# Optimization experiments

Measured on AMD Instinct MI355X. Metric: run time of the kernel, lower is better.

Reference implementation:

```python
import jax, jax.numpy as jnp
import numpy as np

L, B, E = 2048, 4, 1024
H = 8
D1 = 2048          # expand_ratio * E, multiple of H
HD = D1 // H       # head dim 256
MAX_L = 2048
EPS = 1e-8


def setup_inputs() -> dict:
    key = jax.random.key(0)
    ks = jax.random.split(key, 9)
    std = 0.02
    return {
        "x": jax.random.normal(ks[0], (L, B, E), jnp.float32),
        "Wu": jax.random.normal(ks[1], (D1, E), jnp.float32) * std,
        "bu": jax.random.normal(ks[2], (D1,), jnp.float32) * std,
        "Wv": jax.random.normal(ks[3], (D1, E), jnp.float32) * std,
        "bv": jax.random.normal(ks[4], (D1,), jnp.float32) * std,
        "Wo": jax.random.normal(ks[5], (E, D1), jnp.float32) * std,
        "bo": jax.random.normal(ks[6], (E,), jnp.float32) * std,
        "zero": jax.random.normal(ks[7], (H, 1), jnp.float32) * 0.1,   # Toeplitz coef, offset 0
        "pos": jax.random.normal(ks[8], (H, MAX_L - 1), jnp.float32) * 0.1,  # offsets 1..n-1
    }


def _simple_rmsnorm(x):
    d = x.shape[-1]
    rms = jnp.linalg.norm(x, axis=-1, keepdims=True) * (d ** -0.5)
    return x / (rms + EPS)


def _toeplitz_causal_fft(v, zero, pos):
    # v: (b, h, n, hd); causal Toeplitz mixing along n via FFT long conv
    n = v.shape[-2]
    coef = jnp.concatenate([zero, pos[:, : n - 1]], axis=-1)  # (h, n)
    m = 2 * n
    cf = jnp.fft.rfft(coef, m, axis=-1)                  # (h, m//2+1)
    vf = jnp.fft.rfft(v, m, axis=-2)                     # (b, h, m//2+1, hd)
    out = jnp.fft.irfft(cf[None, :, :, None] * vf, m, axis=-2)
    return out[:, :, :n, :]


def reference(x, Wu, bu, Wv, bv, Wo, bo, zero, pos):
    # x: (n, b, e) fairseq layout
    n, b, e = x.shape
    shortcut = x
    xn = _simple_rmsnorm(x)                               # pre_norm (SimpleRMSNorm, no params)
    u = jax.nn.silu(jnp.einsum('nbe,de->nbd', xn, Wu) + bu)   # (n,b,d1)
    v = jax.nn.silu(jnp.einsum('nbe,de->nbd', xn, Wv) + bv)   # (n,b,d1)
    # 'n b (h d) -> b h n d'
    vh = v.transpose(1, 0, 2).reshape(b, n, H, HD).transpose(0, 2, 1, 3)
    oh = _toeplitz_causal_fft(vh, zero, pos)              # (b,h,n,hd)
    o = oh.transpose(0, 2, 1, 3).reshape(b, n, D1).transpose(1, 0, 2)  # (n,b,d1)
    o = u * o                                             # gating
    out = jnp.einsum('nbd,ed->nbe', o, Wo) + bo + shortcut
    return out
```

## Files before the change

kernel.cpp:

```cpp
#include <hip/hip_runtime.h>
#include <cstdint>
#include <cstddef>

#define LQ   2048
#define BQ   4
#define EQ   1024
#define HQ   8
#define D1Q  2048
#define HDQ  256
#define NBQ  (LQ*BQ)

typedef __bf16 bf16_t;
typedef __bf16 bf16x8 __attribute__((ext_vector_type(8)));
typedef __bf16 bf16x4 __attribute__((ext_vector_type(4)));
typedef float  f32x4  __attribute__((ext_vector_type(4)));

#define GAS1(p) ((const __attribute__((address_space(1))) void*)(p))
#define LAS3(p) ((__attribute__((address_space(3))) void*)(p))


__global__ __launch_bounds__(256) void convert_kernel(
    const float* __restrict__ Wu, const float* __restrict__ Wv,
    const float* __restrict__ Wo,
    bf16_t* __restrict__ Wub, bf16_t* __restrict__ Wvb,
    bf16_t* __restrict__ Wob)
{
    const size_t i = (size_t)blockIdx.x * 256 + threadIdx.x;
    if (i < (size_t)D1Q * EQ) {
        Wub[i] = (bf16_t)Wu[i];
        Wvb[i] = (bf16_t)Wv[i];
        Wob[i] = (bf16_t)Wo[i];
    }
}

__global__ __launch_bounds__(256) void build_toep_tiles(
    const float* __restrict__ zero, const float* __restrict__ pos,
    bf16_t* __restrict__ Atiles)
{
    const int q = blockIdx.x;
    const int h = blockIdx.y;
    const int doff = (q - 3) * 32;
    const int tid = threadIdx.x;
    bf16_t* dst = Atiles + ((size_t)h * 64 + q) * (128 * 32);
    const int e0 = tid * 16;
    const int r = e0 >> 5;
    const int cbase = e0 & 31;
    bf16_t vals[16];
    #pragma unroll
    for (int j = 0; j < 16; ++j) {
        const int d = doff + r - (cbase + j);
        float v = 0.f;
        if (d == 0) v = zero[h];
        else if (d > 0) v = pos[(size_t)h * (LQ - 1) + d - 1];
        vals[j] = (bf16_t)v;
    }
    *(bf16x8*)(dst + e0)     = *(bf16x8*)(vals);
    *(bf16x8*)(dst + e0 + 8) = *(bf16x8*)(vals + 8);
}

__global__ __launch_bounds__(256) void rmsnorm_kernel(
    const float* __restrict__ x, bf16_t* __restrict__ xn)
{
    const int row = blockIdx.x;
    const int tid = threadIdx.x;
    const float4 v = ((const float4*)(x + (size_t)row * EQ))[tid];
    float ss = v.x*v.x + v.y*v.y + v.z*v.z + v.w*v.w;
    #pragma unroll
    for (int m = 32; m >= 1; m >>= 1) ss += __shfl_xor(ss, m, 64);
    __shared__ float red[4];
    const int wid = tid >> 6, lane = tid & 63;
    if (lane == 0) red[wid] = ss;
    __syncthreads();
    const float tot = red[0] + red[1] + red[2] + red[3];
    const float inv = 1.f / (sqrtf(tot * (1.f / EQ)) + 1e-8f);
    bf16x4 o;
    o[0] = (bf16_t)(v.x * inv); o[1] = (bf16_t)(v.y * inv);
    o[2] = (bf16_t)(v.z * inv); o[3] = (bf16_t)(v.w * inv);
    *(bf16x4*)(xn + (size_t)row * EQ + tid * 4) = o;
}

__global__ __launch_bounds__(512, 4) void gemm_uv(
    const bf16_t* __restrict__ A, const bf16_t* __restrict__ Bm,
    const float* __restrict__ bbu, const float* __restrict__ bbv,
    bf16_t* __restrict__ Ub, bf16_t* __restrict__ Vt)
{
    constexpr int K = EQ;
    constexpr int BUF = 24576;
    __shared__ alignas(16) char smem[2 * BUF];

    const int nwg   = gridDim.x * gridDim.y;
    const int bid0  = blockIdx.y * gridDim.x + blockIdx.x;
    const int chunkw = nwg >> 3;
    const int sb    = (bid0 & 7) * chunkw + (bid0 >> 3);
    const int bx    = sb % gridDim.x;
    const int by    = sb / gridDim.x;

    const int tid  = threadIdx.x;
    const int wid  = tid >> 6;
    const int lane = tid & 63;
    const int frow = lane & 15;
    const int c    = lane >> 4;
    const int m0 = by * 256;
    const int n0 = bx * 128;
    const int wm = wid >> 1, wn = wid & 1;
    const int wrm = wm * 64, wrn = wn * 64;

    const int g = (frow >> 1) & 3;
    const int offA0 = (wrm + frow) * 64 + ((c ^ g) << 4);
    const int offB0 = 16384 + (wrn + frow) * 64 + ((c ^ g) << 4);

    const int rA   = tid >> 2;
    const int soff = (((tid & 3) ^ ((rA >> 1) & 3)) << 4);
    const size_t lda2 = (size_t)K * 2;
    const char* sA = (const char*)A  + (size_t)(m0 + rA) * lda2 + soff;
    const char* sB = (const char*)Bm + (size_t)(n0 + rA) * lda2 + soff;

    auto STAGE = [&](int bf, int kt) {
        char* dA = smem + bf * BUF + wid * 1024;
        __builtin_amdgcn_global_load_lds(GAS1(sA + (size_t)kt * 64), LAS3(dA), 16, 0, 0);
        __builtin_amdgcn_global_load_lds(GAS1(sA + 128 * lda2 + (size_t)kt * 64),
                                         LAS3(dA + 8192), 16, 0, 0);
        char* dB = smem + bf * BUF + 16384 + wid * 1024;
        __builtin_amdgcn_global_load_lds(GAS1(sB + (size_t)kt * 64), LAS3(dB), 16, 0, 0);
    };

    f32x4 acc[4][4];
    #pragma unroll
    for (int i = 0; i < 4; ++i)
        #pragma unroll
        for (int j = 0; j < 4; ++j) acc[i][j] = (f32x4){0.f, 0.f, 0.f, 0.f};

    const int NT = K >> 5;

    STAGE(0, 0);
    asm volatile("s_waitcnt vmcnt(0)" ::: "memory");
    __builtin_amdgcn_s_barrier();

    for (int t = 0; t < NT; ++t) {
        if (t + 1 < NT) STAGE((t + 1) & 1, t + 1);
        const char* base = smem + (t & 1) * BUF;
        bf16x8 av[4], bv[4];
        #pragma unroll
        for (int i = 0; i < 4; ++i) {
            av[i] = *(const bf16x8*)(base + offA0 + i * 1024);
            bv[i] = *(const bf16x8*)(base + offB0 + i * 1024);
        }
        __builtin_amdgcn_s_setprio(1);
        #pragma unroll
        for (int mi = 0; mi < 4; ++mi)
            #pragma unroll
            for (int ni = 0; ni < 4; ++ni)
                acc[mi][ni] = __builtin_amdgcn_mfma_f32_16x16x32_bf16(
                    av[mi], bv[ni], acc[mi][ni], 0, 0, 0);
        __builtin_amdgcn_s_setprio(0);
        asm volatile("s_waitcnt vmcnt(0)" ::: "memory");
        __builtin_amdgcn_s_barrier();
    }

    if (bx < 16) {
        const int fq = c * 4;
        #pragma unroll
        for (int mi = 0; mi < 4; ++mi) {
            #pragma unroll
            for (int ni = 0; ni < 4; ++ni) {
                const int gn = n0 + wrn + ni * 16 + frow;
                #pragma unroll
                for (int j = 0; j < 4; ++j) {
                    const int gm = m0 + wrm + mi * 16 + fq + j;
                    float v = acc[mi][ni][j] + bbu[gn];
                    v = v / (1.f + __expf(-v));
                    Ub[(size_t)gm * D1Q + gn] = (bf16_t)v;
                }
            }
        }
        return;
    }

    {
        const int n0v = n0 - 2048;
        const int hh  = n0v >> 8;
        const int hdb = (n0v & 255) + wrn;
        float bb[4];
        #pragma unroll
        for (int ni = 0; ni < 4; ++ni) bb[ni] = bbv[n0v + wrn + ni * 16 + frow];

        bf16_t* chunk = (bf16_t*)smem + wn * 8448;
        #pragma unroll
        for (int p = 0; p < 2; ++p) {
            __syncthreads();
            #pragma unroll
            for (int mi = 0; mi < 4; ++mi) {
                #pragma unroll
                for (int nio = 0; nio < 2; ++nio) {
                    const int ni = p * 2 + nio;
                    const int nl = nio * 16 + frow;
                    const int tl = wm * 16 + mi * 4 + c;
                    #pragma unroll
                    for (int j = 0; j < 4; ++j) {
                        float v = acc[mi][ni][j] + bb[ni];
                        v = v / (1.f + __expf(-v));
                        chunk[nl * 264 + j * 64 + tl] = (bf16_t)v;
                    }
                }
            }
            __syncthreads();
            const int nl    = lane & 31;
            const int thalf = lane >> 5;
            const int b2    = wm;
            const int hd    = hdb + p * 32 + nl;
            const int t0    = (m0 >> 2) + thalf * 32;
            const bf16_t* src = chunk + nl * 264 + b2 * 64 + thalf * 32;
            bf16_t* dst = Vt + (((size_t)hh * 4 + b2) * 256 + hd) * (size_t)LQ + t0;
            #pragma unroll
            for (int u = 0; u < 4; ++u)
                *(bf16x8*)(dst + u * 8) = *(const bf16x8*)(src + u * 8);
        }
    }
}

__global__ __launch_bounds__(256, 4) void gemm_toep(
    const bf16_t* __restrict__ VT, const bf16_t* __restrict__ Atiles,
    const bf16_t* __restrict__ U, bf16_t* __restrict__ O)
{
    constexpr int BUF = 16384;
    __shared__ alignas(16) char smem[2 * BUF];

    const int bid   = blockIdx.x;
    const int m_blk = 15 - (bid >> 6);
    const int sub   = bid & 63;
    const int h     = sub >> 3;
    const int n0    = (sub & 7) * 128;
    const int m0    = m_blk * 128;

    const int tid  = threadIdx.x;
    const int wid  = tid >> 6;
    const int lane = tid & 63;
    const int frow = lane & 15;
    const int c    = lane >> 4;
    const int wm = wid >> 1, wn = wid & 1;
    const int wrm = wm * 64, wrn = wn * 64;

    const int g = (frow >> 1) & 3;
    const int offA0 = (wrm + frow) * 64 + ((c ^ g) << 4);
    const int offB0 = 8192 + (wrn + frow) * 64 + ((c ^ g) << 4);

    const int rA   = tid >> 2;
    const int soff = (((tid & 3) ^ ((rA >> 1) & 3)) << 4);
    const char* Ah = (const char*)Atiles + (size_t)h * 64 * 8192;
    const size_t ldb = (size_t)LQ * 2;
    const char* sB = (const char*)VT + ((size_t)h * 1024 + n0 + rA) * ldb + soff;

    auto STAGE = [&](int bf, int kt) {
        const int q = 4 * m_blk + 3 - kt;
        const char* s = Ah + (size_t)q * 8192 + (size_t)rA * 64 + soff;
        char* dA = smem + bf * BUF + wid * 1024;
        __builtin_amdgcn_global_load_lds(GAS1(s), LAS3(dA), 16, 0, 0);
        __builtin_amdgcn_global_load_lds(GAS1(s + 4096), LAS3(dA + 4096), 16, 0, 0);
        char* dB = smem + bf * BUF + 8192 + wid * 1024;
        __builtin_amdgcn_global_load_lds(GAS1(sB + (size_t)kt * 64), LAS3(dB), 16, 0, 0);
        __builtin_amdgcn_global_load_lds(GAS1(sB + 64 * ldb + (size_t)kt * 64),
                                         LAS3(dB + 4096), 16, 0, 0);
    };

    f32x4 acc[4][4];
    #pragma unroll
    for (int i = 0; i < 4; ++i)
        #pragma unroll
        for (int j = 0; j < 4; ++j) acc[i][j] = (f32x4){0.f, 0.f, 0.f, 0.f};

    const int NT = 4 * m_blk + 4;

    STAGE(0, 0);
    asm volatile("s_waitcnt vmcnt(0)" ::: "memory");
    __builtin_amdgcn_s_barrier();

    for (int t = 0; t < NT; ++t) {
        if (t + 1 < NT) STAGE((t + 1) & 1, t + 1);
        const char* base = smem + (t & 1) * BUF;
        bf16x8 av[4], bv[4];
        #pragma unroll
        for (int i = 0; i < 4; ++i) {
            av[i] = *(const bf16x8*)(base + offA0 + i * 1024);
            bv[i] = *(const bf16x8*)(base + offB0 + i * 1024);
        }
        __builtin_amdgcn_s_setprio(1);
        #pragma unroll
        for (int mi = 0; mi < 4; ++mi)
            #pragma unroll
            for (int ni = 0; ni < 4; ++ni)
                acc[mi][ni] = __builtin_amdgcn_mfma_f32_16x16x32_bf16(
                    av[mi], bv[ni], acc[mi][ni], 0, 0, 0);
        __builtin_amdgcn_s_setprio(0);
        asm volatile("s_waitcnt vmcnt(0)" ::: "memory");
        __builtin_amdgcn_s_barrier();
    }

    const int fq = c * 4;
    #pragma unroll
    for (int mi = 0; mi < 4; ++mi) {
        #pragma unroll
        for (int ni = 0; ni < 4; ++ni) {
            const int nn = n0 + wrn + ni * 16 + frow;
            const int b  = nn >> 8, hd = nn & 255;
            #pragma unroll
            for (int j = 0; j < 4; ++j) {
                const int t = m0 + wrm + mi * 16 + fq + j;
                const size_t idx = ((size_t)t * BQ + b) * D1Q + h * HDQ + hd;
                const float uval = (float)U[idx];
                O[idx] = (bf16_t)(uval * acc[mi][ni][j]);
            }
        }
    }
}

__global__ __launch_bounds__(256, 4) void gemm_fin(
    const bf16_t* __restrict__ A, const bf16_t* __restrict__ Bm,
    const float* __restrict__ bias, const float* __restrict__ res,
    float* __restrict__ Cf)
{
    constexpr int K = D1Q, N = EQ;
    constexpr int BUF = 16384;
    __shared__ alignas(16) char smem[2 * BUF];

    const int nwg   = gridDim.x * gridDim.y;
    const int bid0  = blockIdx.y * gridDim.x + blockIdx.x;
    const int chunkw = nwg >> 3;
    const int sb    = (bid0 & 7) * chunkw + (bid0 >> 3);
    const int bx    = sb % gridDim.x;
    const int by    = sb / gridDim.x;

    const int tid  = threadIdx.x;
    const int wid  = tid >> 6;
    const int lane = tid & 63;
    const int frow = lane & 15;
    const int c    = lane >> 4;
    const int m0 = by * 128;
    const int n0 = bx * 128;
    const int wm = wid >> 1, wn = wid & 1;
    const int wrm = wm * 64, wrn = wn * 64;

    const int g = (frow >> 1) & 3;
    const int offA0 = (wrm + frow) * 64 + ((c ^ g) << 4);
    const int offB0 = 8192 + (wrn + frow) * 64 + ((c ^ g) << 4);

    const int rA   = tid >> 2;
    const int soff = (((tid & 3) ^ ((rA >> 1) & 3)) << 4);
    const size_t lda2 = (size_t)K * 2;
    const char* sA = (const char*)A  + (size_t)(m0 + rA) * lda2 + soff;
    const char* sB = (const char*)Bm + (size_t)(n0 + rA) * lda2 + soff;

    auto STAGE = [&](int bf, int kt) {
        char* dA = smem + bf * BUF + wid * 1024;
        __builtin_amdgcn_global_load_lds(GAS1(sA + (size_t)kt * 64), LAS3(dA), 16, 0, 0);
        __builtin_amdgcn_global_load_lds(GAS1(sA + 64 * lda2 + (size_t)kt * 64),
                                         LAS3(dA + 4096), 16, 0, 0);
        char* dB = smem + bf * BUF + 8192 + wid * 1024;
        __builtin_amdgcn_global_load_lds(GAS1(sB + (size_t)kt * 64), LAS3(dB), 16, 0, 0);
        __builtin_amdgcn_global_load_lds(GAS1(sB + 64 * lda2 + (size_t)kt * 64),
                                         LAS3(dB + 4096), 16, 0, 0);
    };

    f32x4 acc[4][4];
    #pragma unroll
    for (int i = 0; i < 4; ++i)
        #pragma unroll
        for (int j = 0; j < 4; ++j) acc[i][j] = (f32x4){0.f, 0.f, 0.f, 0.f};

    const int NT = K >> 5;

    STAGE(0, 0);
    asm volatile("s_waitcnt vmcnt(0)" ::: "memory");
    __builtin_amdgcn_s_barrier();

    for (int t = 0; t < NT; ++t) {
        if (t + 1 < NT) STAGE((t + 1) & 1, t + 1);
        const char* base = smem + (t & 1) * BUF;
        bf16x8 av[4], bv[4];
        #pragma unroll
        for (int i = 0; i < 4; ++i) {
            av[i] = *(const bf16x8*)(base + offA0 + i * 1024);
            bv[i] = *(const bf16x8*)(base + offB0 + i * 1024);
        }
        __builtin_amdgcn_s_setprio(1);
        #pragma unroll
        for (int mi = 0; mi < 4; ++mi)
            #pragma unroll
            for (int ni = 0; ni < 4; ++ni)
                acc[mi][ni] = __builtin_amdgcn_mfma_f32_16x16x32_bf16(
                    av[mi], bv[ni], acc[mi][ni], 0, 0, 0);
        __builtin_amdgcn_s_setprio(0);
        asm volatile("s_waitcnt vmcnt(0)" ::: "memory");
        __builtin_amdgcn_s_barrier();
    }

    const int fq = c * 4;
    #pragma unroll
    for (int mi = 0; mi < 4; ++mi) {
        #pragma unroll
        for (int ni = 0; ni < 4; ++ni) {
            const int gn = n0 + wrn + ni * 16 + frow;
            #pragma unroll
            for (int j = 0; j < 4; ++j) {
                const int gm = m0 + wrm + mi * 16 + fq + j;
                Cf[(size_t)gm * N + gn] =
                    acc[mi][ni][j] + bias[gn] + res[(size_t)gm * N + gn];
            }
        }
    }
}


extern "C" void kernel_launch(void* const* d_in, const int* in_sizes, int n_in,
                              void* d_out, int out_size, void* d_ws, size_t ws_size,
                              hipStream_t stream)
{
    const float* x    = (const float*)d_in[0];
    const float* Wu   = (const float*)d_in[1];
    const float* bu   = (const float*)d_in[2];
    const float* Wv   = (const float*)d_in[3];
    const float* bv   = (const float*)d_in[4];
    const float* Wo   = (const float*)d_in[5];
    const float* bo   = (const float*)d_in[6];
    const float* zero = (const float*)d_in[7];
    const float* pos  = (const float*)d_in[8];
    float* out = (float*)d_out;

    char* ws = (char*)d_ws;
    size_t off = 0;
    auto alloc = [&](size_t bytes) {
        char* p = ws + off;
        off += (bytes + 255) & ~(size_t)255;
        return p;
    };
    bf16_t* xn     = (bf16_t*)alloc((size_t)NBQ * EQ * 2);
    bf16_t* Wub    = (bf16_t*)alloc((size_t)D1Q * EQ * 2);
    bf16_t* Wvb    = (bf16_t*)alloc((size_t)D1Q * EQ * 2);
    bf16_t* Wob    = (bf16_t*)alloc((size_t)EQ * D1Q * 2);
    bf16_t* Atiles = (bf16_t*)alloc((size_t)HQ * 64 * 4096 * 2);
    bf16_t* Ub     = (bf16_t*)alloc((size_t)NBQ * D1Q * 2);
    bf16_t* VTb    = (bf16_t*)alloc((size_t)NBQ * D1Q * 2);
    bf16_t* Ob     = (bf16_t*)alloc((size_t)NBQ * D1Q * 2);

    convert_kernel<<<8192, 256, 0, stream>>>(Wu, Wv, Wo, Wub, Wvb, Wob);
    build_toep_tiles<<<dim3(64, 8), 256, 0, stream>>>(zero, pos, Atiles);
    rmsnorm_kernel<<<NBQ, 256, 0, stream>>>(x, xn);

    dim3 g1(32, NBQ / 256);
    gemm_uv<<<g1, 512, 0, stream>>>(xn, Wub, bu, bv, Ub, VTb);

    gemm_toep<<<1024, 256, 0, stream>>>(VTb, Atiles, Ub, Ob);

    dim3 g2(EQ / 128, NBQ / 128);
    gemm_fin<<<g2, 256, 0, stream>>>(Ob, Wob, bo, x, out);
}
```

Before: 200.2 us.

## Triple-buffer GEMM pipelines, enlarge toep/fin tiles, vectorize weight conversion

All three GEMMs move from double to triple-buffered LDS staging, keeping two tiles in flight so global loads overlap more of the MFMA work. The Toeplitz and final GEMMs switch to 512-thread blocks with 128x256 and 256x128 tiles. This halves their grid sizes and raises data reuse per block, at the cost of fewer blocks and higher LDS use per CU. The weight conversion kernel now processes four floats per thread with vector loads and stores.

After: 198.4 us, median of 3. Within noise of the previous version (-0.9%).

```diff
diff --git a/kernel.cpp b/kernel.cpp
--- a/kernel.cpp
+++ b/kernel.cpp
@@ -25,11 +25,18 @@
     bf16_t* __restrict__ Wub, bf16_t* __restrict__ Wvb,
     bf16_t* __restrict__ Wob)
 {
-    const size_t i = (size_t)blockIdx.x * 256 + threadIdx.x;
+    const size_t i = ((size_t)blockIdx.x * 256 + threadIdx.x) * 4;
     if (i < (size_t)D1Q * EQ) {
-        Wub[i] = (bf16_t)Wu[i];
-        Wvb[i] = (bf16_t)Wv[i];
-        Wob[i] = (bf16_t)Wo[i];
+        float4 a = *(const float4*)(Wu + i);
+        float4 b = *(const float4*)(Wv + i);
+        float4 d = *(const float4*)(Wo + i);
+        bf16x4 oa, ob, od;
+        oa[0]=(bf16_t)a.x; oa[1]=(bf16_t)a.y; oa[2]=(bf16_t)a.z; oa[3]=(bf16_t)a.w;
+        ob[0]=(bf16_t)b.x; ob[1]=(bf16_t)b.y; ob[2]=(bf16_t)b.z; ob[3]=(bf16_t)b.w;
+        od[0]=(bf16_t)d.x; od[1]=(bf16_t)d.y; od[2]=(bf16_t)d.z; od[3]=(bf16_t)d.w;
+        *(bf16x4*)(Wub + i) = oa;
+        *(bf16x4*)(Wvb + i) = ob;
+        *(bf16x4*)(Wob + i) = od;
     }
 }
 
@@ -79,14 +86,15 @@
     *(bf16x4*)(xn + (size_t)row * EQ + tid * 4) = o;
 }
 
-__global__ __launch_bounds__(512, 4) void gemm_uv(
+
+__global__ __launch_bounds__(512, 2) void gemm_uv(
     const bf16_t* __restrict__ A, const bf16_t* __restrict__ Bm,
     const float* __restrict__ bbu, const float* __restrict__ bbv,
     bf16_t* __restrict__ Ub, bf16_t* __restrict__ Vt)
 {
     constexpr int K = EQ;
     constexpr int BUF = 24576;
-    __shared__ alignas(16) char smem[2 * BUF];
+    __shared__ alignas(16) char smem[3 * BUF];
 
     const int nwg   = gridDim.x * gridDim.y;
     const int bid0  = blockIdx.y * gridDim.x + blockIdx.x;
@@ -132,13 +140,14 @@
 
     const int NT = K >> 5;
 
-    STAGE(0, 0);
-    asm volatile("s_waitcnt vmcnt(0)" ::: "memory");
+    STAGE(0, 0); STAGE(1, 1);
+    asm volatile("s_waitcnt vmcnt(3)" ::: "memory");
     __builtin_amdgcn_s_barrier();
 
+    int cur = 0, pb = 2;
     for (int t = 0; t < NT; ++t) {
-        if (t + 1 < NT) STAGE((t + 1) & 1, t + 1);
-        const char* base = smem + (t & 1) * BUF;
+        if (t + 2 < NT) STAGE(pb, t + 2);
+        const char* base = smem + cur * BUF;
         bf16x8 av[4], bv[4];
         #pragma unroll
         for (int i = 0; i < 4; ++i) {
@@ -153,8 +162,13 @@
                 acc[mi][ni] = __builtin_amdgcn_mfma_f32_16x16x32_bf16(
                     av[mi], bv[ni], acc[mi][ni], 0, 0, 0);
         __builtin_amdgcn_s_setprio(0);
-        asm volatile("s_waitcnt vmcnt(0)" ::: "memory");
-        __builtin_amdgcn_s_barrier();
+        if (t + 1 < NT) {
+            if (t + 2 < NT) asm volatile("s_waitcnt vmcnt(3)" ::: "memory");
+            else            asm volatile("s_waitcnt vmcnt(0)" ::: "memory");
+            __builtin_amdgcn_s_barrier();
+        }
+        cur = (cur == 2) ? 0 : cur + 1;
+        pb  = (pb  == 2) ? 0 : pb  + 1;
     }
 
     if (bx < 16) {
@@ -218,18 +232,18 @@
     }
 }
 
-__global__ __launch_bounds__(256, 4) void gemm_toep(
+__global__ __launch_bounds__(512, 2) void gemm_toep(
     const bf16_t* __restrict__ VT, const bf16_t* __restrict__ Atiles,
     const bf16_t* __restrict__ U, bf16_t* __restrict__ O)
 {
-    constexpr int BUF = 16384;
-    __shared__ alignas(16) char smem[2 * BUF];
+    constexpr int BUF = 24576;
+    __shared__ alignas(16) char smem[3 * BUF];
 
     const int bid   = blockIdx.x;
-    const int m_blk = 15 - (bid >> 6);
-    const int sub   = bid & 63;
-    const int h     = sub >> 3;
-    const int n0    = (sub & 7) * 128;
+    const int m_blk = 15 - (bid >> 5);
+    const int sub   = bid & 31;
+    const int h     = sub >> 2;
+    const int n0    = (sub & 3) * 256;
     const int m0    = m_blk * 128;
 
     const int tid  = threadIdx.x;
@@ -237,8 +251,8 @@
     const int lane = tid & 63;
     const int frow = lane & 15;
     const int c    = lane >> 4;
-    const int wm = wid >> 1, wn = wid & 1;
-    const int wrm = wm * 64, wrn = wn * 64;
+    const int wrm  = (wid >> 2) * 64;
+    const int wrn  = (wid & 3) * 64;
 
     const int g = (frow >> 1) & 3;
     const int offA0 = (wrm + frow) * 64 + ((c ^ g) << 4);
@@ -253,13 +267,12 @@
     auto STAGE = [&](int bf, int kt) {
         const int q = 4 * m_blk + 3 - kt;
         const char* s = Ah + (size_t)q * 8192 + (size_t)rA * 64 + soff;
-        char* dA = smem + bf * BUF + wid * 1024;
-        __builtin_amdgcn_global_load_lds(GAS1(s), LAS3(dA), 16, 0, 0);
-        __builtin_amdgcn_global_load_lds(GAS1(s + 4096), LAS3(dA + 4096), 16, 0, 0);
+        __builtin_amdgcn_global_load_lds(GAS1(s),
+                                         LAS3(smem + bf * BUF + wid * 1024), 16, 0, 0);
         char* dB = smem + bf * BUF + 8192 + wid * 1024;
         __builtin_amdgcn_global_load_lds(GAS1(sB + (size_t)kt * 64), LAS3(dB), 16, 0, 0);
-        __builtin_amdgcn_global_load_lds(GAS1(sB + 64 * ldb + (size_t)kt * 64),
-                                         LAS3(dB + 4096), 16, 0, 0);
+        __builtin_amdgcn_global_load_lds(GAS1(sB + 128 * ldb + (size_t)kt * 64),
+                                         LAS3(dB + 8192), 16, 0, 0);
     };
 
     f32x4 acc[4][4];
@@ -270,13 +283,14 @@
 
     const int NT = 4 * m_blk + 4;
 
-    STAGE(0, 0);
-    asm volatile("s_waitcnt vmcnt(0)" ::: "memory");
+    STAGE(0, 0); STAGE(1, 1);
+    asm volatile("s_waitcnt vmcnt(3)" ::: "memory");
     __builtin_amdgcn_s_barrier();
 
+    int cur = 0, pb = 2;
     for (int t = 0; t < NT; ++t) {
-        if (t + 1 < NT) STAGE((t + 1) & 1, t + 1);
-        const char* base = smem + (t & 1) * BUF;
+        if (t + 2 < NT) STAGE(pb, t + 2);
+        const char* base = smem + cur * BUF;
         bf16x8 av[4], bv[4];
         #pragma unroll
         for (int i = 0; i < 4; ++i) {
@@ -291,8 +305,13 @@
                 acc[mi][ni] = __builtin_amdgcn_mfma_f32_16x16x32_bf16(
                     av[mi], bv[ni], acc[mi][ni], 0, 0, 0);
         __builtin_amdgcn_s_setprio(0);
-        asm volatile("s_waitcnt vmcnt(0)" ::: "memory");
-        __builtin_amdgcn_s_barrier();
+        if (t + 1 < NT) {
+            if (t + 2 < NT) asm volatile("s_waitcnt vmcnt(3)" ::: "memory");
+            else            asm volatile("s_waitcnt vmcnt(0)" ::: "memory");
+            __builtin_amdgcn_s_barrier();
+        }
+        cur = (cur == 2) ? 0 : cur + 1;
+        pb  = (pb  == 2) ? 0 : pb  + 1;
     }
 
     const int fq = c * 4;
@@ -313,14 +332,14 @@
     }
 }
 
-__global__ __launch_bounds__(256, 4) void gemm_fin(
+__global__ __launch_bounds__(512, 2) void gemm_fin(
     const bf16_t* __restrict__ A, const bf16_t* __restrict__ Bm,
     const float* __restrict__ bias, const float* __restrict__ res,
     float* __restrict__ Cf)
 {
     constexpr int K = D1Q, N = EQ;
-    constexpr int BUF = 16384;
-    __shared__ alignas(16) char smem[2 * BUF];
+    constexpr int BUF = 24576;
+    __shared__ alignas(16) char smem[3 * BUF];
 
     const int nwg   = gridDim.x * gridDim.y;
     const int bid0  = blockIdx.y * gridDim.x + blockIdx.x;
@@ -334,14 +353,14 @@
     const int lane = tid & 63;
     const int frow = lane & 15;
     const int c    = lane >> 4;
-    const int m0 = by * 128;
+    const int m0 = by * 256;
     const int n0 = bx * 128;
     const int wm = wid >> 1, wn = wid & 1;
     const int wrm = wm * 64, wrn = wn * 64;
 
     const int g = (frow >> 1) & 3;
     const int offA0 = (wrm + frow) * 64 + ((c ^ g) << 4);
-    const int offB0 = 8192 + (wrn + frow) * 64 + ((c ^ g) << 4);
+    const int offB0 = 16384 + (wrn + frow) * 64 + ((c ^ g) << 4);
 
     const int rA   = tid >> 2;
     const int soff = (((tid & 3) ^ ((rA >> 1) & 3)) << 4);
@@ -352,12 +371,10 @@
     auto STAGE = [&](int bf, int kt) {
         char* dA = smem + bf * BUF + wid * 1024;
         __builtin_amdgcn_global_load_lds(GAS1(sA + (size_t)kt * 64), LAS3(dA), 16, 0, 0);
-        __builtin_amdgcn_global_load_lds(GAS1(sA + 64 * lda2 + (size_t)kt * 64),
-                                         LAS3(dA + 4096), 16, 0, 0);
-        char* dB = smem + bf * BUF + 8192 + wid * 1024;
+        __builtin_amdgcn_global_load_lds(GAS1(sA + 128 * lda2 + (size_t)kt * 64),
+                                         LAS3(dA + 8192), 16, 0, 0);
+        char* dB = smem + bf * BUF + 16384 + wid * 1024;
         __builtin_amdgcn_global_load_lds(GAS1(sB + (size_t)kt * 64), LAS3(dB), 16, 0, 0);
-        __builtin_amdgcn_global_load_lds(GAS1(sB + 64 * lda2 + (size_t)kt * 64),
-                                         LAS3(dB + 4096), 16, 0, 0);
     };
 
     f32x4 acc[4][4];
@@ -368,13 +385,14 @@
 
     const int NT = K >> 5;
 
-    STAGE(0, 0);
-    asm volatile("s_waitcnt vmcnt(0)" ::: "memory");
+    STAGE(0, 0); STAGE(1, 1);
+    asm volatile("s_waitcnt vmcnt(3)" ::: "memory");
     __builtin_amdgcn_s_barrier();
 
+    int cur = 0, pb = 2;
     for (int t = 0; t < NT; ++t) {
-        if (t + 1 < NT) STAGE((t + 1) & 1, t + 1);
-        const char* base = smem + (t & 1) * BUF;
+        if (t + 2 < NT) STAGE(pb, t + 2);
+        const char* base = smem + cur * BUF;
         bf16x8 av[4], bv[4];
         #pragma unroll
         for (int i = 0; i < 4; ++i) {
@@ -389,8 +407,13 @@
                 acc[mi][ni] = __builtin_amdgcn_mfma_f32_16x16x32_bf16(
                     av[mi], bv[ni], acc[mi][ni], 0, 0, 0);
         __builtin_amdgcn_s_setprio(0);
-        asm volatile("s_waitcnt vmcnt(0)" ::: "memory");
-        __builtin_amdgcn_s_barrier();
+        if (t + 1 < NT) {
+            if (t + 2 < NT) asm volatile("s_waitcnt vmcnt(3)" ::: "memory");
+            else            asm volatile("s_waitcnt vmcnt(0)" ::: "memory");
+            __builtin_amdgcn_s_barrier();
+        }
+        cur = (cur == 2) ? 0 : cur + 1;
+        pb  = (pb  == 2) ? 0 : pb  + 1;
     }
 
     const int fq = c * 4;
@@ -441,15 +464,15 @@
     bf16_t* VTb    = (bf16_t*)alloc((size_t)NBQ * D1Q * 2);
     bf16_t* Ob     = (bf16_t*)alloc((size_t)NBQ * D1Q * 2);
 
-    convert_kernel<<<8192, 256, 0, stream>>>(Wu, Wv, Wo, Wub, Wvb, Wob);
+    convert_kernel<<<2048, 256, 0, stream>>>(Wu, Wv, Wo, Wub, Wvb, Wob);
     build_toep_tiles<<<dim3(64, 8), 256, 0, stream>>>(zero, pos, Atiles);
     rmsnorm_kernel<<<NBQ, 256, 0, stream>>>(x, xn);
 
     dim3 g1(32, NBQ / 256);
     gemm_uv<<<g1, 512, 0, stream>>>(xn, Wub, bu, bv, Ub, VTb);
 
-    gemm_toep<<<1024, 256, 0, stream>>>(VTb, Atiles, Ub, Ob);
-
-    dim3 g2(EQ / 128, NBQ / 128);
-    gemm_fin<<<g2, 256, 0, stream>>>(Ob, Wob, bo, x, out);
-}
+    gemm_toep<<<512, 512, 0, stream>>>(VTb, Atiles, Ub, Ob);
+
+    dim3 g2(EQ / 128, NBQ / 256);
+    gemm_fin<<<g2, 512, 0, stream>>>(Ob, Wob, bo, x, out);
+}
```
